# Performance work log

Measured on AMD Instinct MI355X. Metric: run time of the kernel, lower is better.

The kernel has to match this reference:

```python
import jax, jax.numpy as jnp
import numpy as np

N, E, F, ED, L = 10000, 640000, 128, 16, 2
EPS = 1e-05


def setup_inputs() -> dict:
    key = jax.random.key(0)
    ks = jax.random.split(key, 12)
    x = jax.random.normal(ks[0], (N, F), dtype=jnp.float32)
    edge_index = jax.random.randint(ks[1], (E, 2), 0, N, dtype=jnp.int64)
    edge_feature = jax.random.normal(ks[2], (E, ED), dtype=jnp.float32)
    edge_weight = jnp.ones((E,), dtype=jnp.float32)
    deg_hist = jax.random.randint(ks[3], (64,), 0, 100, dtype=jnp.int64)
    s = 0.05
    edge_enc_w = jax.random.normal(ks[4], (L, ED, F), dtype=jnp.float32) * s
    edge_enc_b = jnp.zeros((L, F), dtype=jnp.float32)
    pre_w = jax.random.normal(ks[5], (L, 3 * F, F), dtype=jnp.float32) * s
    pre_b = jnp.zeros((L, F), dtype=jnp.float32)
    post_w = jax.random.normal(ks[6], (L, 13 * F, F), dtype=jnp.float32) * s
    post_b = jnp.zeros((L, F), dtype=jnp.float32)
    upd_w = jax.random.normal(ks[7], (L, F, F), dtype=jnp.float32) * s
    upd_b = jnp.zeros((L, F), dtype=jnp.float32)
    return {"x": x, "edge_feature": edge_feature, "edge_weight": edge_weight,
            "edge_enc_w": edge_enc_w, "edge_enc_b": edge_enc_b,
            "pre_w": pre_w, "pre_b": pre_b, "post_w": post_w, "post_b": post_b,
            "upd_w": upd_w, "upd_b": upd_b,
            "edge_index": edge_index, "deg_hist": deg_hist}


def _pna_forward(x, edge_feature, edge_weight, edge_enc_w, edge_enc_b,
                 pre_w, pre_b, post_w, post_b, upd_w, upd_b,
                 src, dst, deg_hist):
    # avg-degree statistics from the degree histogram (constants of the layer)
    dh = deg_hist.astype(jnp.float32)
    bins = jnp.arange(dh.shape[0], dtype=jnp.float32)
    avg_log = jnp.sum(jnp.log(bins + 1.0) * dh) / jnp.sum(dh)

    # in-degree of destination nodes
    deg = jax.ops.segment_sum(jnp.ones((src.shape[0],), x.dtype), dst, num_segments=N)  # [N]
    safe_deg = jnp.maximum(deg, 1.0)[:, None]
    log_deg = jnp.log(deg + 1.0)
    amp = (log_deg / avg_log)[:, None]                                   # amplification scale
    att = jnp.where(deg == 0, 1.0, avg_log / jnp.where(deg == 0, 1.0, log_deg))[:, None]
    has_nb = (deg > 0)[:, None]

    h = x
    for l in range(L):
        # pre-MLP on [h_src | h_dst | edge_attr]: split the concat matmul into 3 GEMMs
        ea = edge_feature @ edge_enc_w[l] + edge_enc_b[l]                # [E, F]
        w_src, w_dst, w_ea = pre_w[l, :F], pre_w[l, F:2 * F], pre_w[l, 2 * F:]
        m = (h @ w_src)[src] + (h @ w_dst)[dst] + ea @ w_ea + pre_b[l]  # [E, F]
        m = m * edge_weight[:, None]

        # multi-aggregator scatter reduce over dst
        s = jax.ops.segment_sum(m, dst, num_segments=N)
        mean = s / safe_deg
        mn = jnp.where(has_nb, jax.ops.segment_min(m, dst, num_segments=N), 0.0)
        mx = jnp.where(has_nb, jax.ops.segment_max(m, dst, num_segments=N), 0.0)
        mean_sq = jax.ops.segment_sum(m * m, dst, num_segments=N) / safe_deg
        var = mean_sq - mean * mean
        std = jnp.sqrt(jax.nn.relu(var) + EPS)
        agg = jnp.concatenate([mean, mn, mx, std], axis=-1)              # [N, 4F]

        # degree scalers: identity, amplification, attenuation
        upd = jnp.concatenate([agg, agg * amp, agg * att], axis=-1)      # [N, 12F]

        # post-MLP on [input | update], then update_mlp
        out = jnp.concatenate([h, upd], axis=-1) @ post_w[l] + post_b[l]
        h = out @ upd_w[l] + upd_b[l]
    return h


def reference(x, edge_feature, edge_weight, edge_enc_w, edge_enc_b,
              pre_w, pre_b, post_w, post_b, upd_w, upd_b,
              edge_index, deg_hist):
    src = edge_index[:, 0]
    dst = edge_index[:, 1]
    return _pna_forward(x, edge_feature, edge_weight, edge_enc_w, edge_enc_b,
                        pre_w, pre_b, post_w, post_b, upd_w, upd_b,
                        src, dst, deg_hist)
```

## Files before the change

kernel.cpp:

```cpp
#include <hip/hip_runtime.h>
#include <hip/hip_bf16.h>
#include <math.h>

#define NN 10000
#define EE 640000
#define FF 128
#define KSPLIT 13

__global__ __launch_bounds__(64) void avglog_k(const int* __restrict__ dh,
                                               float* __restrict__ out) {
  int t = threadIdx.x;
  float v = (float)dh[t];
  float num = logf((float)t + 1.0f) * v;
#pragma unroll
  for (int off = 32; off > 0; off >>= 1) {
    num += __shfl_down(num, off);
    v   += __shfl_down(v, off);
  }
  if (t == 0) out[0] = num / v;
}

__global__ __launch_bounds__(256) void count_k(const int* __restrict__ ei,
                                               int* __restrict__ cnt, int E) {
  int e = blockIdx.x * 256 + threadIdx.x;
  if (e < E) {
    int d = ei[2 * (size_t)e + 1];
    atomicAdd(&cnt[d], 1);
  }
}

__global__ __launch_bounds__(1024) void scan_k(const int* __restrict__ cnt,
                                               int* __restrict__ offs,
                                               int* __restrict__ cursor, int n) {
  __shared__ int sh[1024];
  __shared__ int carry_s;
  int tid = threadIdx.x;
  if (tid == 0) carry_s = 0;
  __syncthreads();
  for (int base = 0; base < n; base += 1024) {
    int i = base + tid;
    int v = (i < n) ? cnt[i] : 0;
    sh[tid] = v;
    __syncthreads();
#pragma unroll
    for (int off = 1; off < 1024; off <<= 1) {
      int add = (tid >= off) ? sh[tid - off] : 0;
      __syncthreads();
      sh[tid] += add;
      __syncthreads();
    }
    int incl = sh[tid];
    int carry = carry_s;
    int excl = carry + incl - v;
    if (i < n) { offs[i] = excl; cursor[i] = excl; }
    int tot = sh[1023];
    __syncthreads();
    if (tid == 0) carry_s = carry + tot;
    __syncthreads();
  }
  if (tid == 0) offs[n] = carry_s;
}

__global__ __launch_bounds__(256) void scatter_k(const int* __restrict__ ei,
                                                 int* __restrict__ cursor,
                                                 int* __restrict__ src_sorted,
                                                 int* __restrict__ eid_sorted, int E) {
  int e = blockIdx.x * 256 + threadIdx.x;
  if (e < E) {
    int d = ei[2 * (size_t)e + 1];
    int p = atomicAdd(&cursor[d], 1);
    src_sorted[p] = ei[2 * (size_t)e];
    eid_sorted[p] = e;
  }
}

__global__ __launch_bounds__(256) void wcomb_k(const float* __restrict__ enc_w,
                                               const float* __restrict__ enc_b,
                                               const float* __restrict__ w_ea,
                                               const float* __restrict__ pre_b,
                                               float* __restrict__ Wc,
                                               float* __restrict__ bc) {
  int o = blockIdx.x * 256 + threadIdx.x;
  if (o < 16 * 128) {
    int k = o >> 7, j = o & 127;
    float acc = 0.f;
    for (int c = 0; c < 128; ++c) acc += enc_w[k * 128 + c] * w_ea[c * 128 + j];
    Wc[o] = acc;
  } else if (o < 16 * 128 + 128) {
    int j = o - 2048;
    float acc = pre_b[j];
    for (int c = 0; c < 128; ++c) acc += enc_b[c] * w_ea[c * 128 + j];
    bc[j] = acc;
  }
}

__global__ __launch_bounds__(128) void gemm_k(const float* __restrict__ A, int lda, int Klen,
                                              const float* __restrict__ B,
                                              const float* __restrict__ bias,
                                              float* __restrict__ C, int M) {
  __shared__ float As[32][36];
  __shared__ float Bs[32][128];
  int tid = threadIdx.x;
  int kc = blockIdx.y;
  const float* Ab = A + (size_t)kc * Klen;
  const float* Bb = B + (size_t)kc * Klen * 128;
  float* Cb = C + (size_t)kc * (size_t)M * 128;
  int row0 = blockIdx.x * 32;
  int tc = tid & 15;
  int tr = tid >> 4;
  int la_r = tid >> 2;
  int la_k = (tid & 3) << 3;
  int lb_c = (tid & 31) << 2;
  int lb_r = tid >> 5;
  float acc[4][8] = {{0.f}};

  int ar = row0 + la_r;
  if (ar >= M) ar = M - 1;
  const float* Ap = Ab + (size_t)ar * lda + la_k;

  for (int k0 = 0; k0 < Klen; k0 += 32) {
    float4 av0 = *(const float4*)(Ap + k0);
    float4 av1 = *(const float4*)(Ap + k0 + 4);
    *(float4*)&As[la_r][la_k]     = av0;
    *(float4*)&As[la_r][la_k + 4] = av1;
#pragma unroll
    for (int p = 0; p < 8; ++p) {
      int bk = lb_r + (p << 2);
      *(float4*)&Bs[bk][lb_c] = *(const float4*)(Bb + (size_t)(k0 + bk) * 128 + lb_c);
    }
    __syncthreads();
#pragma unroll
    for (int kk = 0; kk < 32; kk += 4) {
      __align__(16) float a[4][4];
#pragma unroll
      for (int r = 0; r < 4; ++r)
        *(float4*)&a[r][0] = *(const float4*)&As[tr * 4 + r][kk];
#pragma unroll
      for (int j = 0; j < 4; ++j) {
        float4 b0 = *(const float4*)&Bs[kk + j][tc << 2];
        float4 b1 = *(const float4*)&Bs[kk + j][64 + (tc << 2)];
#pragma unroll
        for (int r = 0; r < 4; ++r) {
          float av = a[r][j];
          acc[r][0] += av * b0.x; acc[r][1] += av * b0.y;
          acc[r][2] += av * b0.z; acc[r][3] += av * b0.w;
          acc[r][4] += av * b1.x; acc[r][5] += av * b1.y;
          acc[r][6] += av * b1.z; acc[r][7] += av * b1.w;
        }
      }
    }
    __syncthreads();
  }

  float4 bb0 = make_float4(0.f, 0.f, 0.f, 0.f);
  float4 bb1 = bb0;
  if (bias) {
    bb0 = *(const float4*)(bias + (tc << 2));
    bb1 = *(const float4*)(bias + 64 + (tc << 2));
  }
#pragma unroll
  for (int r = 0; r < 4; ++r) {
    int row = row0 + tr * 4 + r;
    if (row < M) {
      float4 v0 = make_float4(acc[r][0] + bb0.x, acc[r][1] + bb0.y,
                              acc[r][2] + bb0.z, acc[r][3] + bb0.w);
      float4 v1 = make_float4(acc[r][4] + bb1.x, acc[r][5] + bb1.y,
                              acc[r][6] + bb1.z, acc[r][7] + bb1.w);
      *(float4*)(Cb + (size_t)row * 128 + (tc << 2)) = v0;
      *(float4*)(Cb + (size_t)row * 128 + 64 + (tc << 2)) = v1;
    }
  }
}

__global__ __launch_bounds__(256) void reduceS_k(const float* __restrict__ part,
                                                 const float* __restrict__ bias,
                                                 float* __restrict__ C) {
  int i = blockIdx.x * 256 + threadIdx.x;
  const int S = NN * 128;
  float v = bias[i & 127];
#pragma unroll
  for (int p = 0; p < KSPLIT; ++p) v += part[i + (size_t)p * S];
  C[i] = v;
}

__global__ __launch_bounds__(128) void agg_k(const float* __restrict__ h,
                                             const float* __restrict__ hs,
                                             const float* __restrict__ hd,
                                             const float* __restrict__ ef,
                                             const float* __restrict__ ew,
                                             const int* __restrict__ offs,
                                             const int* __restrict__ src_sorted,
                                             const int* __restrict__ eid_sorted,
                                             const float* __restrict__ Wc,
                                             const float* __restrict__ bc,
                                             const float* __restrict__ avg_log_p,
                                             float* __restrict__ Amat) {
  __shared__ int sbuf[128];
  __shared__ int ibuf[128];
  int n = blockIdx.x;
  int t = threadIdx.x;

  float wc[16];
#pragma unroll
  for (int k = 0; k < 16; ++k) wc[k] = Wc[k * 128 + t];

  float base = hd[(size_t)n * 128 + t] + bc[t];
  int e0 = offs[n], e1 = offs[n + 1];

  float sum = 0.f, sq = 0.f;
  float mn = 3.402823466e38f, mx = -3.402823466e38f;

  for (int c0 = e0; c0 < e1; c0 += 128) {
    int cN = e1 - c0; if (cN > 128) cN = 128;
    __syncthreads();
    if (t < cN) {
      sbuf[t] = src_sorted[c0 + t];
      ibuf[t] = eid_sorted[c0 + t];
    }
    __syncthreads();
#pragma unroll 2
    for (int i = 0; i < cN; ++i) {
      int s = sbuf[i], id = ibuf[i];
      float hv = hs[(size_t)s * 128 + t];
      float w = ew[id];
      const float4* efp = (const float4*)(ef + (size_t)id * 16);
      float4 f0 = efp[0], f1 = efp[1], f2 = efp[2], f3 = efp[3];
      float m = base + hv;
      m += f0.x * wc[0]  + f0.y * wc[1]  + f0.z * wc[2]  + f0.w * wc[3];
      m += f1.x * wc[4]  + f1.y * wc[5]  + f1.z * wc[6]  + f1.w * wc[7];
      m += f2.x * wc[8]  + f2.y * wc[9]  + f2.z * wc[10] + f2.w * wc[11];
      m += f3.x * wc[12] + f3.y * wc[13] + f3.z * wc[14] + f3.w * wc[15];
      m *= w;
      sum += m;
      sq  += m * m;
      mn = fminf(mn, m);
      mx = fmaxf(mx, m);
    }
  }

  int deg = e1 - e0;
  float fdeg = (float)deg;
  float safe = fmaxf(fdeg, 1.f);
  float mean = sum / safe;
  float var = sq / safe - mean * mean;
  float stdv = sqrtf(fmaxf(var, 0.f) + 1e-5f);
  if (deg == 0) { mn = 0.f; mx = 0.f; }

  float avg_log = avg_log_p[0];
  float logd = logf(fdeg + 1.f);
  float amp = logd / avg_log;
  float att = (deg == 0) ? 1.f : (avg_log / logd);

  float* row = Amat + (size_t)n * 1664;
  row[t] = h[(size_t)n * 128 + t];
  float a0 = mean, a1 = mn, a2 = mx, a3 = stdv;
  row[128 + t] = a0;  row[256 + t] = a1;  row[384 + t] = a2;  row[512 + t] = a3;
  row[640 + t] = a0 * amp;  row[768 + t] = a1 * amp;  row[896 + t] = a2 * amp;  row[1024 + t] = a3 * amp;
  row[1152 + t] = a0 * att; row[1280 + t] = a1 * att; row[1408 + t] = a2 * att; row[1536 + t] = a3 * att;
}

extern "C" void kernel_launch(void* const* d_in, const int* in_sizes, int n_in,
                              void* d_out, int out_size, void* d_ws, size_t ws_size,
                              hipStream_t stream) {
  (void)in_sizes; (void)n_in; (void)out_size; (void)ws_size;
  const float* x      = (const float*)d_in[0];
  const float* ef     = (const float*)d_in[1];
  const float* ew     = (const float*)d_in[2];
  const float* enc_w  = (const float*)d_in[3];
  const float* enc_b  = (const float*)d_in[4];
  const float* pre_w  = (const float*)d_in[5];
  const float* pre_b  = (const float*)d_in[6];
  const float* post_w = (const float*)d_in[7];
  const float* post_b = (const float*)d_in[8];
  const float* upd_w  = (const float*)d_in[9];
  const float* upd_b  = (const float*)d_in[10];
  const int* ei       = (const int*)d_in[11];
  const int* dh       = (const int*)d_in[12];

  char* ws = (char*)d_ws;
  size_t off = 0;
  auto alloc = [&](size_t bytes) -> void* {
    void* p = ws + off;
    off += (bytes + 255) & ~(size_t)255;
    return p;
  };
  float* avg_log    = (float*)alloc(4);
  int*   cnt        = (int*)alloc(NN * 4);
  int*   offs       = (int*)alloc((NN + 1) * 4);
  int*   cursor     = (int*)alloc(NN * 4);
  int*   src_sorted = (int*)alloc((size_t)EE * 4);
  int*   eid_sorted = (int*)alloc((size_t)EE * 4);
  float* Wc         = (float*)alloc(16 * 128 * 4);
  float* bc         = (float*)alloc(128 * 4);
  float* hs         = (float*)alloc((size_t)NN * 128 * 4);
  float* hd         = (float*)alloc((size_t)NN * 128 * 4);
  float* hbuf       = (float*)alloc((size_t)NN * 128 * 4);
  float* outb       = (float*)alloc((size_t)NN * 128 * 4);
  float* Cpart      = (float*)alloc((size_t)KSPLIT * NN * 128 * 4);
  float* Amat       = (float*)alloc((size_t)NN * 1664 * 4);

  hipMemsetAsync(cnt, 0, NN * 4, stream);
  avglog_k<<<1, 64, 0, stream>>>(dh, avg_log);
  count_k<<<(EE + 255) / 256, 256, 0, stream>>>(ei, cnt, EE);
  scan_k<<<1, 1024, 0, stream>>>(cnt, offs, cursor, NN);
  scatter_k<<<(EE + 255) / 256, 256, 0, stream>>>(ei, cursor, src_sorted, eid_sorted, EE);

  const int gx = (NN + 31) / 32;
  const float* h = x;
  for (int l = 0; l < 2; ++l) {
    const float* wl = pre_w + (size_t)l * 384 * 128;
    wcomb_k<<<9, 256, 0, stream>>>(enc_w + (size_t)l * 16 * 128, enc_b + l * 128,
                                   wl + 256 * 128, pre_b + l * 128, Wc, bc);
    gemm_k<<<dim3(gx, 1), 128, 0, stream>>>(h, 128, 128, wl, nullptr, hs, NN);
    gemm_k<<<dim3(gx, 1), 128, 0, stream>>>(h, 128, 128, wl + 128 * 128, nullptr, hd, NN);
    agg_k<<<NN, 128, 0, stream>>>(h, hs, hd, ef, ew, offs, src_sorted, eid_sorted,
                                  Wc, bc, avg_log, Amat);
    gemm_k<<<dim3(gx, KSPLIT), 128, 0, stream>>>(Amat, 1664, 128,
                                                 post_w + (size_t)l * 1664 * 128,
                                                 nullptr, Cpart, NN);
    reduceS_k<<<(NN * 128) / 256, 256, 0, stream>>>(Cpart, post_b + l * 128, outb);
    float* hn = (l == 0) ? hbuf : (float*)d_out;
    gemm_k<<<dim3(gx, 1), 128, 0, stream>>>(outb, 128, 128,
                                            upd_w + (size_t)l * 128 * 128,
                                            upd_b + l * 128, hn, NN);
    h = hbuf;
  }
}
```

Before: 696.3 us.

## Factor degree scalers out of post-MLP GEMM and restructure aggregation

Rather than building a 1664-wide row holding the identity, amp and att scaled copies, the post-MLP is rewritten algebraically. The 512-wide aggregate is multiplied by three repacked weight slices, and the results are combined per node with the amp and att scalars, which shrinks that GEMM K by roughly a factor of three. The h-input part of the post weights is fused with the two pre-MLP projections into one 384-wide GEMM. Edge features and weights are pre-sorted by destination during the CSR scatter so the aggregation reads them contiguously. The aggregation now splits each node's edges over 4 warp groups with a shared-memory reduction, and the prefix scan becomes a single-pass blocked scan. The cost is extra packing kernels and larger sorted-copy buffers.

```diff
diff --git a/kernel.cpp b/kernel.cpp
--- a/kernel.cpp
+++ b/kernel.cpp
@@ -5,7 +5,7 @@
 #define NN 10000
 #define EE 640000
 #define FF 128
-#define KSPLIT 13
+#define KS 2
 
 __global__ __launch_bounds__(64) void avglog_k(const int* __restrict__ dh,
                                                float* __restrict__ out) {
@@ -33,44 +33,51 @@
                                                int* __restrict__ offs,
                                                int* __restrict__ cursor, int n) {
   __shared__ int sh[1024];
-  __shared__ int carry_s;
   int tid = threadIdx.x;
-  if (tid == 0) carry_s = 0;
+  int lex[10];
+  int i0 = tid * 10;
+  int s = 0;
+#pragma unroll
+  for (int k = 0; k < 10; ++k) {
+    int i = i0 + k;
+    int v = (i < n) ? cnt[i] : 0;
+    lex[k] = s;
+    s += v;
+  }
+  sh[tid] = s;
   __syncthreads();
-  for (int base = 0; base < n; base += 1024) {
-    int i = base + tid;
-    int v = (i < n) ? cnt[i] : 0;
-    sh[tid] = v;
+#pragma unroll
+  for (int off = 1; off < 1024; off <<= 1) {
+    int add = (tid >= off) ? sh[tid - off] : 0;
     __syncthreads();
-#pragma unroll
-    for (int off = 1; off < 1024; off <<= 1) {
-      int add = (tid >= off) ? sh[tid - off] : 0;
-      __syncthreads();
-      sh[tid] += add;
-      __syncthreads();
-    }
-    int incl = sh[tid];
-    int carry = carry_s;
-    int excl = carry + incl - v;
-    if (i < n) { offs[i] = excl; cursor[i] = excl; }
-    int tot = sh[1023];
+    sh[tid] += add;
     __syncthreads();
-    if (tid == 0) carry_s = carry + tot;
-    __syncthreads();
-  }
-  if (tid == 0) offs[n] = carry_s;
+  }
+  int base = (tid == 0) ? 0 : sh[tid - 1];
+#pragma unroll
+  for (int k = 0; k < 10; ++k) {
+    int i = i0 + k;
+    if (i < n) { int e = base + lex[k]; offs[i] = e; cursor[i] = e; }
+  }
+  if (tid == 1023) offs[n] = sh[1023];
 }
 
 __global__ __launch_bounds__(256) void scatter_k(const int* __restrict__ ei,
                                                  int* __restrict__ cursor,
                                                  int* __restrict__ src_sorted,
-                                                 int* __restrict__ eid_sorted, int E) {
+                                                 const float* __restrict__ ef,
+                                                 const float* __restrict__ ew,
+                                                 float* __restrict__ ef_s,
+                                                 float* __restrict__ ew_s, int E) {
   int e = blockIdx.x * 256 + threadIdx.x;
   if (e < E) {
     int d = ei[2 * (size_t)e + 1];
     int p = atomicAdd(&cursor[d], 1);
     src_sorted[p] = ei[2 * (size_t)e];
-    eid_sorted[p] = e;
+    ew_s[p] = ew[e];
+    const float4* s4 = (const float4*)(ef + (size_t)e * 16);
+    float4* d4 = (float4*)(ef_s + (size_t)p * 16);
+    d4[0] = s4[0]; d4[1] = s4[1]; d4[2] = s4[2]; d4[3] = s4[3];
   }
 }
 
@@ -94,17 +101,36 @@
   }
 }
 
+__global__ __launch_bounds__(256) void bpack_k(const float* __restrict__ pw,
+                                               const float* __restrict__ wl,
+                                               float* __restrict__ Bp,
+                                               float* __restrict__ B3) {
+  int idx = blockIdx.x * 256 + threadIdx.x;
+  if (idx < 512 * 384) {
+    int k = idx / 384, c = idx - k * 384;
+    int p = c >> 7, j = c & 127;
+    Bp[idx] = pw[(size_t)(128 + p * 512 + k) * 128 + j];
+  } else if (idx < 512 * 384 + 128 * 384) {
+    int r = idx - 512 * 384;
+    int k = r / 384, c = r - k * 384;
+    int p = c >> 7, j = c & 127;
+    const float* srcm = (p == 0) ? wl : (p == 1 ? wl + 128 * 128 : pw);
+    B3[r] = srcm[k * 128 + j];
+  }
+}
+
 __global__ __launch_bounds__(128) void gemm_k(const float* __restrict__ A, int lda, int Klen,
-                                              const float* __restrict__ B,
+                                              const float* __restrict__ B, int ldb,
                                               const float* __restrict__ bias,
-                                              float* __restrict__ C, int M) {
+                                              float* __restrict__ C, int ldc, int M) {
   __shared__ float As[32][36];
   __shared__ float Bs[32][128];
   int tid = threadIdx.x;
   int kc = blockIdx.y;
+  int col0 = blockIdx.z << 7;
   const float* Ab = A + (size_t)kc * Klen;
-  const float* Bb = B + (size_t)kc * Klen * 128;
-  float* Cb = C + (size_t)kc * (size_t)M * 128;
+  const float* Bb = B + (size_t)kc * Klen * ldb + col0;
+  float* Cb = C + (size_t)kc * (size_t)M * ldc + col0;
   int row0 = blockIdx.x * 32;
   int tc = tid & 15;
   int tr = tid >> 4;
@@ -126,7 +152,7 @@
 #pragma unroll
     for (int p = 0; p < 8; ++p) {
       int bk = lb_r + (p << 2);
-      *(float4*)&Bs[bk][lb_c] = *(const float4*)(Bb + (size_t)(k0 + bk) * 128 + lb_c);
+      *(float4*)&Bs[bk][lb_c] = *(const float4*)(Bb + (size_t)(k0 + bk) * ldb + lb_c);
     }
     __syncthreads();
 #pragma unroll
@@ -155,8 +181,8 @@
   float4 bb0 = make_float4(0.f, 0.f, 0.f, 0.f);
   float4 bb1 = bb0;
   if (bias) {
-    bb0 = *(const float4*)(bias + (tc << 2));
-    bb1 = *(const float4*)(bias + 64 + (tc << 2));
+    bb0 = *(const float4*)(bias + col0 + (tc << 2));
+    bb1 = *(const float4*)(bias + col0 + 64 + (tc << 2));
   }
 #pragma unroll
   for (int r = 0; r < 4; ++r) {
@@ -166,97 +192,106 @@
                               acc[r][2] + bb0.z, acc[r][3] + bb0.w);
       float4 v1 = make_float4(acc[r][4] + bb1.x, acc[r][5] + bb1.y,
                               acc[r][6] + bb1.z, acc[r][7] + bb1.w);
-      *(float4*)(Cb + (size_t)row * 128 + (tc << 2)) = v0;
-      *(float4*)(Cb + (size_t)row * 128 + 64 + (tc << 2)) = v1;
+      *(float4*)(Cb + (size_t)row * ldc + (tc << 2)) = v0;
+      *(float4*)(Cb + (size_t)row * ldc + 64 + (tc << 2)) = v1;
     }
   }
 }
 
-__global__ __launch_bounds__(256) void reduceS_k(const float* __restrict__ part,
-                                                 const float* __restrict__ bias,
-                                                 float* __restrict__ C) {
+__global__ __launch_bounds__(256) void finp_k(const float* __restrict__ Cpart,
+                                              const float* __restrict__ hsd,
+                                              const float* __restrict__ ampv,
+                                              const float* __restrict__ attv,
+                                              const float* __restrict__ bias,
+                                              float* __restrict__ out) {
   int i = blockIdx.x * 256 + threadIdx.x;
-  const int S = NN * 128;
-  float v = bias[i & 127];
-#pragma unroll
-  for (int p = 0; p < KSPLIT; ++p) v += part[i + (size_t)p * S];
-  C[i] = v;
-}
-
-__global__ __launch_bounds__(128) void agg_k(const float* __restrict__ h,
-                                             const float* __restrict__ hs,
-                                             const float* __restrict__ hd,
-                                             const float* __restrict__ ef,
-                                             const float* __restrict__ ew,
+  int n = i >> 7, j = i & 127;
+  const size_t S = (size_t)NN * 384;
+  float g1 = 0.f, g2 = 0.f, g3 = 0.f;
+#pragma unroll
+  for (int kc = 0; kc < KS; ++kc) {
+    const float* r = Cpart + kc * S + (size_t)n * 384;
+    g1 += r[j]; g2 += r[128 + j]; g3 += r[256 + j];
+  }
+  out[i] = hsd[(size_t)n * 384 + 256 + j] + g1 + ampv[n] * g2 + attv[n] * g3 + bias[j];
+}
+
+__global__ __launch_bounds__(512) void agg_k(const float* __restrict__ hsd,
+                                             const float* __restrict__ ef_s,
+                                             const float* __restrict__ ew_s,
                                              const int* __restrict__ offs,
                                              const int* __restrict__ src_sorted,
-                                             const int* __restrict__ eid_sorted,
                                              const float* __restrict__ Wc,
                                              const float* __restrict__ bc,
                                              const float* __restrict__ avg_log_p,
-                                             float* __restrict__ Amat) {
-  __shared__ int sbuf[128];
-  __shared__ int ibuf[128];
+                                             float* __restrict__ AggM,
+                                             float* __restrict__ ampv,
+                                             float* __restrict__ attv) {
+  __shared__ float red[4][4][128];
   int n = blockIdx.x;
   int t = threadIdx.x;
+  int g = t >> 7;
+  int f = t & 127;
 
   float wc[16];
 #pragma unroll
-  for (int k = 0; k < 16; ++k) wc[k] = Wc[k * 128 + t];
-
-  float base = hd[(size_t)n * 128 + t] + bc[t];
+  for (int k = 0; k < 16; ++k) wc[k] = Wc[k * 128 + f];
+
+  float base = hsd[(size_t)n * 384 + 128 + f] + bc[f];
   int e0 = offs[n], e1 = offs[n + 1];
 
   float sum = 0.f, sq = 0.f;
   float mn = 3.402823466e38f, mx = -3.402823466e38f;
 
-  for (int c0 = e0; c0 < e1; c0 += 128) {
-    int cN = e1 - c0; if (cN > 128) cN = 128;
-    __syncthreads();
-    if (t < cN) {
-      sbuf[t] = src_sorted[c0 + t];
-      ibuf[t] = eid_sorted[c0 + t];
+#pragma unroll 2
+  for (int e = e0 + g; e < e1; e += 4) {
+    int s = src_sorted[e];
+    float w = ew_s[e];
+    const float4* efp = (const float4*)(ef_s + (size_t)e * 16);
+    float4 f0 = efp[0], f1 = efp[1], f2 = efp[2], f3 = efp[3];
+    float m = base + hsd[(size_t)s * 384 + f];
+    m += f0.x * wc[0]  + f0.y * wc[1]  + f0.z * wc[2]  + f0.w * wc[3];
+    m += f1.x * wc[4]  + f1.y * wc[5]  + f1.z * wc[6]  + f1.w * wc[7];
+    m += f2.x * wc[8]  + f2.y * wc[9]  + f2.z * wc[10] + f2.w * wc[11];
+    m += f3.x * wc[12] + f3.y * wc[13] + f3.z * wc[14] + f3.w * wc[15];
+    m *= w;
+    sum += m;
+    sq  += m * m;
+    mn = fminf(mn, m);
+    mx = fmaxf(mx, m);
+  }
+
+  red[0][g][f] = sum; red[1][g][f] = sq; red[2][g][f] = mn; red[3][g][f] = mx;
+  __syncthreads();
+  {
+    int s = g;
+    float a = red[s][0][f], b = red[s][1][f], c = red[s][2][f], d = red[s][3][f];
+    float r;
+    if (s < 2)       r = (a + b) + (c + d);
+    else if (s == 2) r = fminf(fminf(a, b), fminf(c, d));
+    else             r = fmaxf(fmaxf(a, b), fmaxf(c, d));
+    red[s][0][f] = r;
+  }
+  __syncthreads();
+  if (t < 128) {
+    float s_  = red[0][0][t], q_ = red[1][0][t];
+    float mn_ = red[2][0][t], mx_ = red[3][0][t];
+    int deg = e1 - e0;
+    float fdeg = (float)deg;
+    float safe = fmaxf(fdeg, 1.f);
+    float mean = s_ / safe;
+    float var = q_ / safe - mean * mean;
+    float stdv = sqrtf(fmaxf(var, 0.f) + 1e-5f);
+    if (deg == 0) { mn_ = 0.f; mx_ = 0.f; }
+    float* row = AggM + (size_t)n * 512;
+    row[t] = mean; row[128 + t] = mn_; row[256 + t] = mx_; row[384 + t] = stdv;
+    if (t == 0) {
+      float avg = avg_log_p[0];
+      float ld = logf(fdeg + 1.f);
+      ampv[n] = ld / avg;
+      attv[n] = (deg == 0) ? 1.f : (avg / ld);
     }
-    __syncthreads();
-#pragma unroll 2
-    for (int i = 0; i < cN; ++i) {
-      int s = sbuf[i], id = ibuf[i];
-      float hv = hs[(size_t)s * 128 + t];
-      float w = ew[id];
-      const float4* efp = (const float4*)(ef + (size_t)id * 16);
-      float4 f0 = efp[0], f1 = efp[1], f2 = efp[2], f3 = efp[3];
-      float m = base + hv;
-      m += f0.x * wc[0]  + f0.y * wc[1]  + f0.z * wc[2]  + f0.w * wc[3];
-      m += f1.x * wc[4]  + f1.y * wc[5]  + f1.z * wc[6]  + f1.w * wc[7];
-      m += f2.x * wc[8]  + f2.y * wc[9]  + f2.z * wc[10] + f2.w * wc[11];
-      m += f3.x * wc[12] + f3.y * wc[13] + f3.z * wc[14] + f3.w * wc[15];
-      m *= w;
-      sum += m;
-      sq  += m * m;
-      mn = fminf(mn, m);
-      mx = fmaxf(mx, m);
-    }
-  }
-
-  int deg = e1 - e0;
-  float fdeg = (float)deg;
-  float safe = fmaxf(fdeg, 1.f);
-  float mean = sum / safe;
-  float var = sq / safe - mean * mean;
-  float stdv = sqrtf(fmaxf(var, 0.f) + 1e-5f);
-  if (deg == 0) { mn = 0.f; mx = 0.f; }
-
-  float avg_log = avg_log_p[0];
-  float logd = logf(fdeg + 1.f);
-  float amp = logd / avg_log;
-  float att = (deg == 0) ? 1.f : (avg_log / logd);
-
-  float* row = Amat + (size_t)n * 1664;
-  row[t] = h[(size_t)n * 128 + t];
-  float a0 = mean, a1 = mn, a2 = mx, a3 = stdv;
-  row[128 + t] = a0;  row[256 + t] = a1;  row[384 + t] = a2;  row[512 + t] = a3;
-  row[640 + t] = a0 * amp;  row[768 + t] = a1 * amp;  row[896 + t] = a2 * amp;  row[1024 + t] = a3 * amp;
-  row[1152 + t] = a0 * att; row[1280 + t] = a1 * att; row[1408 + t] = a2 * att; row[1536 + t] = a3 * att;
+  }
 }
 
 extern "C" void kernel_launch(void* const* d_in, const int* in_sizes, int n_in,
@@ -289,40 +324,47 @@
   int*   offs       = (int*)alloc((NN + 1) * 4);
   int*   cursor     = (int*)alloc(NN * 4);
   int*   src_sorted = (int*)alloc((size_t)EE * 4);
-  int*   eid_sorted = (int*)alloc((size_t)EE * 4);
+  float* ef_s       = (float*)alloc((size_t)EE * 16 * 4);
+  float* ew_s       = (float*)alloc((size_t)EE * 4);
   float* Wc         = (float*)alloc(16 * 128 * 4);
   float* bc         = (float*)alloc(128 * 4);
-  float* hs         = (float*)alloc((size_t)NN * 128 * 4);
-  float* hd         = (float*)alloc((size_t)NN * 128 * 4);
+  float* Bpack      = (float*)alloc(512 * 384 * 4);
+  float* B3         = (float*)alloc(128 * 384 * 4);
+  float* hsd        = (float*)alloc((size_t)NN * 384 * 4);
   float* hbuf       = (float*)alloc((size_t)NN * 128 * 4);
   float* outb       = (float*)alloc((size_t)NN * 128 * 4);
-  float* Cpart      = (float*)alloc((size_t)KSPLIT * NN * 128 * 4);
-  float* Amat       = (float*)alloc((size_t)NN * 1664 * 4);
+  float* AggM       = (float*)alloc((size_t)NN * 512 * 4);
+  float* ampv       = (float*)alloc(NN * 4);
+  float* attv       = (float*)alloc(NN * 4);
+  float* Cpart      = (float*)alloc((size_t)KS * NN * 384 * 4);
 
   hipMemsetAsync(cnt, 0, NN * 4, stream);
   avglog_k<<<1, 64, 0, stream>>>(dh, avg_log);
   count_k<<<(EE + 255) / 256, 256, 0, stream>>>(ei, cnt, EE);
   scan_k<<<1, 1024, 0, stream>>>(cnt, offs, cursor, NN);
-  scatter_k<<<(EE + 255) / 256, 256, 0, stream>>>(ei, cursor, src_sorted, eid_sorted, EE);
+  scatter_k<<<(EE + 255) / 256, 256, 0, stream>>>(ei, cursor, src_sorted,
+                                                  ef, ew, ef_s, ew_s, EE);
 
   const int gx = (NN + 31) / 32;
   const float* h = x;
   for (int l = 0; l < 2; ++l) {
     const float* wl = pre_w + (size_t)l * 384 * 128;
+    const float* pw = post_w + (size_t)l * 1664 * 128;
     wcomb_k<<<9, 256, 0, stream>>>(enc_w + (size_t)l * 16 * 128, enc_b + l * 128,
                                    wl + 256 * 128, pre_b + l * 128, Wc, bc);
-    gemm_k<<<dim3(gx, 1), 128, 0, stream>>>(h, 128, 128, wl, nullptr, hs, NN);
-    gemm_k<<<dim3(gx, 1), 128, 0, stream>>>(h, 128, 128, wl + 128 * 128, nullptr, hd, NN);
-    agg_k<<<NN, 128, 0, stream>>>(h, hs, hd, ef, ew, offs, src_sorted, eid_sorted,
-                                  Wc, bc, avg_log, Amat);
-    gemm_k<<<dim3(gx, KSPLIT), 128, 0, stream>>>(Amat, 1664, 128,
-                                                 post_w + (size_t)l * 1664 * 128,
-                                                 nullptr, Cpart, NN);
-    reduceS_k<<<(NN * 128) / 256, 256, 0, stream>>>(Cpart, post_b + l * 128, outb);
+    bpack_k<<<960, 256, 0, stream>>>(pw, wl, Bpack, B3);
+    gemm_k<<<dim3(gx, 1, 3), 128, 0, stream>>>(h, 128, 128, B3, 384,
+                                               nullptr, hsd, 384, NN);
+    agg_k<<<NN, 512, 0, stream>>>(hsd, ef_s, ew_s, offs, src_sorted,
+                                  Wc, bc, avg_log, AggM, ampv, attv);
+    gemm_k<<<dim3(gx, KS, 3), 128, 0, stream>>>(AggM, 512, 512 / KS, Bpack, 384,
+                                                nullptr, Cpart, 384, NN);
+    finp_k<<<(NN * 128) / 256, 256, 0, stream>>>(Cpart, hsd, ampv, attv,
+                                                 post_b + l * 128, outb);
     float* hn = (l == 0) ? hbuf : (float*)d_out;
-    gemm_k<<<dim3(gx, 1), 128, 0, stream>>>(outb, 128, 128,
-                                            upd_w + (size_t)l * 128 * 128,
-                                            upd_b + l * 128, hn, NN);
+    gemm_k<<<dim3(gx, 1, 1), 128, 0, stream>>>(outb, 128, 128,
+                                               upd_w + (size_t)l * 128 * 128, 128,
+                                               upd_b + l * 128, hn, 128, NN);
     h = hbuf;
   }
 }
```

Measured after the change: 791.8 us. +13.7%, slower.
